# Optimization experiments

Hardware: AMD Instinct MI355X
Metric: run time of the kernel (lower is better)

The kernel has to match this reference:

```python
import jax, jax.numpy as jnp
import numpy as np

B, T = 16, 2048
D_EMB, D_CND2, H_RNN, H_FC, N_OUT = 256, 640, 896, 1024, 1024


def setup_inputs() -> dict:
    key = jax.random.key(0)
    ks = jax.random.split(key, 12)
    s = 0.02
    return {
        "reference_sample": jax.random.randint(ks[0], (B, T), 0, N_OUT),
        "i_cnd_series": jax.random.normal(ks[1], (B, T, D_CND2), dtype=jnp.float32),
        "emb": jax.random.normal(ks[2], (N_OUT, D_EMB), dtype=jnp.float32) * s,
        "W_ih": jax.random.normal(ks[3], (3 * H_RNN, D_EMB + D_CND2), dtype=jnp.float32) * s,
        "b_ih": jnp.zeros((3 * H_RNN,), jnp.float32),
        "W_hh": jax.random.normal(ks[4], (3 * H_RNN, H_RNN), dtype=jnp.float32) * s,
        "b_hh": jnp.zeros((3 * H_RNN,), jnp.float32),
        "fc1_w": jax.random.normal(ks[5], (H_FC, H_RNN), dtype=jnp.float32) * s,
        "fc1_b": jnp.zeros((H_FC,), jnp.float32),
        "fc2_w": jax.random.normal(ks[6], (N_OUT, H_FC), dtype=jnp.float32) * s,
        "fc2_b": jnp.zeros((N_OUT,), jnp.float32),
    }


def _gru(x, W_ih, b_ih, W_hh, b_hh):
    # x: [B, T, D_in] -> hidden states [B, T, H] (PyTorch GRU gate order r, z, n)
    Bn = x.shape[0]
    gx = jnp.einsum("btd,gd->btg", x, W_ih) + b_ih  # precompute input gates [B,T,3H]
    gx = jnp.transpose(gx, (1, 0, 2))  # [T,B,3H]

    def step(h, gxt):
        gh = h @ W_hh.T + b_hh
        rx, zx, nx = jnp.split(gxt, 3, axis=-1)
        rh, zh, nh = jnp.split(gh, 3, axis=-1)
        r = jax.nn.sigmoid(rx + rh)
        z = jax.nn.sigmoid(zx + zh)
        n = jnp.tanh(nx + r * nh)
        h_new = (1.0 - z) * n + z * h
        return h_new, h_new

    h0 = jnp.zeros((Bn, W_hh.shape[1]), x.dtype)
    _, hs = jax.lax.scan(step, h0, gx)
    return jnp.transpose(hs, (1, 0, 2))  # [B,T,H]


def reference(reference_sample, i_cnd_series, emb, W_ih, b_ih, W_hh, b_hh,
              fc1_w, fc1_b, fc2_w, fc2_b):
    x_emb = emb[reference_sample]                      # [B,T,D_EMB]
    x = jnp.concatenate([x_emb, i_cnd_series], axis=2)  # [B,T,D_EMB+2*cnd]
    o_rnn = _gru(x, W_ih, b_ih, W_hh, b_hh)            # [B,T,H_RNN]
    h = jax.nn.relu(jnp.einsum("bth,fh->btf", o_rnn, fc1_w) + fc1_b)
    return jnp.einsum("btf,of->bto", h, fc2_w) + fc2_b  # [B,T,N_OUT]
```

## Files before the change

kernel.cpp:

```cpp
#include <hip/hip_runtime.h>
#include <hip/hip_bf16.h>

typedef __bf16 bf16;
typedef __bf16 bf16x2 __attribute__((ext_vector_type(2)));
typedef __bf16 bf16x8 __attribute__((ext_vector_type(8)));
typedef float  floatx4 __attribute__((ext_vector_type(4)));

#define NWG 56

static constexpr size_t FL_OFF  = 0;
static constexpr size_t HB_OFF  = 8192;
static constexpr size_t WBF_OFF = 65536;
static constexpr size_t GX_OFF  = WBF_OFF + 13565952;
static constexpr size_t HSX_OFF = GX_OFF + 176160768;

static constexpr size_t W_IH_E = 2688 * 896;
static constexpr size_t W_HH_E = 2688 * 896;
static constexpr size_t W_F1_E = 1024 * 896;

__device__ __forceinline__ float sigm(float x)      { return 1.f / (1.f + __expf(-x)); }
__device__ __forceinline__ float fast_tanh(float x) { return 2.f / (1.f + __expf(-2.f * x)) - 1.f; }

__global__ __launch_bounds__(256) void k_cvt(const float* __restrict__ src,
                                             bf16* __restrict__ dst)
{
    const int s = blockIdx.x * 256 + threadIdx.x;
    const float4 a = ((const float4*)src)[s * 2 + 0];
    const float4 b = ((const float4*)src)[s * 2 + 1];
    bf16x8 v;
    v[0] = (bf16)a.x; v[1] = (bf16)a.y; v[2] = (bf16)a.z; v[3] = (bf16)a.w;
    v[4] = (bf16)b.x; v[5] = (bf16)b.y; v[6] = (bf16)b.z; v[7] = (bf16)b.w;
    ((bf16x8*)dst)[s] = v;
}

__global__ __launch_bounds__(256) void k_embed(const int* __restrict__ samp,
                                               const float* __restrict__ cnd,
                                               const float* __restrict__ emb,
                                               bf16* __restrict__ x)
{
    const int s = blockIdx.x * 256 + threadIdx.x;
    const int r = s / 112;
    const int c = s % 112;
    const float* src;
    if (c < 32) src = emb + samp[r] * 256 + c * 8;
    else        src = cnd + (long)r * 640 + (c - 32) * 8;
    const float4 a = ((const float4*)src)[0];
    const float4 b = ((const float4*)src)[1];
    bf16x8 v;
    v[0] = (bf16)a.x; v[1] = (bf16)a.y; v[2] = (bf16)a.z; v[3] = (bf16)a.w;
    v[4] = (bf16)b.x; v[5] = (bf16)b.y; v[6] = (bf16)b.z; v[7] = (bf16)b.w;
    *(bf16x8*)(x + (long)r * 896 + c * 8) = v;
}

template <int RELU, int GXMODE, int OUTF32>
__global__ __launch_bounds__(256, 2) void gemm_bt(const bf16* __restrict__ A,
                                                  const bf16* __restrict__ Bw,
                                                  const float* __restrict__ bias,
                                                  void* __restrict__ Cv,
                                                  int M, int N, int K)
{
    __shared__ bf16 As[128 * 40];
    __shared__ bf16 Bs[128 * 40];

    const int tid  = threadIdx.x;
    const int lane = tid & 63;
    const int wv   = tid >> 6;
    const int wm   = wv >> 1;
    const int wn   = wv & 1;
    const int n16  = lane & 15;
    const int quad = lane >> 4;
    const int tm   = blockIdx.y * 128;
    const int tn   = blockIdx.x * 128;

    floatx4 acc[4][4] = {};

    const int s0 = tid, s1 = tid + 256;
    const int r0 = s0 >> 2, c0 = s0 & 3;
    const int r1 = s1 >> 2, c1 = s1 & 3;

    const int KT = K >> 5;
    for (int kt = 0; kt < KT; ++kt) {
        const int k0 = kt * 32;
        bf16x8 a0 = *(const bf16x8*)(A  + (long)(tm + r0) * K + k0 + c0 * 8);
        bf16x8 a1 = *(const bf16x8*)(A  + (long)(tm + r1) * K + k0 + c1 * 8);
        bf16x8 b0 = *(const bf16x8*)(Bw + (long)(tn + r0) * K + k0 + c0 * 8);
        bf16x8 b1 = *(const bf16x8*)(Bw + (long)(tn + r1) * K + k0 + c1 * 8);
        __syncthreads();
        *(bf16x8*)(As + r0 * 40 + c0 * 8) = a0;
        *(bf16x8*)(As + r1 * 40 + c1 * 8) = a1;
        *(bf16x8*)(Bs + r0 * 40 + c0 * 8) = b0;
        *(bf16x8*)(Bs + r1 * 40 + c1 * 8) = b1;
        __syncthreads();

        bf16x8 af[4], bfj[4];
#pragma unroll
        for (int i = 0; i < 4; ++i)
            af[i] = *(const bf16x8*)(As + (wm * 64 + i * 16 + n16) * 40 + quad * 8);
#pragma unroll
        for (int j = 0; j < 4; ++j)
            bfj[j] = *(const bf16x8*)(Bs + (wn * 64 + j * 16 + n16) * 40 + quad * 8);
#pragma unroll
        for (int i = 0; i < 4; ++i)
#pragma unroll
            for (int j = 0; j < 4; ++j)
                acc[i][j] = __builtin_amdgcn_mfma_f32_16x16x32_bf16(af[i], bfj[j], acc[i][j], 0, 0, 0);
    }

#pragma unroll
    for (int j = 0; j < 4; ++j) {
        const int c = tn + wn * 64 + j * 16 + n16;
        const float bv = bias[c];
#pragma unroll
        for (int i = 0; i < 4; ++i) {
            const int rbase = tm + wm * 64 + i * 16 + quad * 4;
#pragma unroll
            for (int rr = 0; rr < 4; ++rr) {
                float v = acc[i][j][rr] + bv;
                if (RELU) v = fmaxf(v, 0.f);
                const int r = rbase + rr;
                long oidx;
                if (GXMODE) { const int tt = r & 2047, bb = r >> 11; oidx = (long)(tt * 16 + bb) * N + c; }
                else        { oidx = (long)r * N + c; }
                if (OUTF32) ((float*)Cv)[oidx] = v;
                else        ((bf16*)Cv)[oidx]  = (bf16)v;
            }
        }
    }
}

__global__ __launch_bounds__(192, 1) void gru_scan(const bf16* __restrict__ Whh,
                                                   const float* __restrict__ bhh,
                                                   const bf16* __restrict__ gx,
                                                   bf16* __restrict__ hs,
                                                   bf16* __restrict__ hbuf,
                                                   unsigned int* __restrict__ flags)
{
    __shared__ bf16  hst[16 * 904];
    __shared__ float gacc[3][16][16];
    __shared__ float bhs[3][16];

    const int tid  = threadIdx.x;
    const int wv   = tid >> 6;
    const int lane = tid & 63;
    const int n16  = lane & 15;
    const int quad = lane >> 4;
    const int wg   = blockIdx.x;
    const int col0 = wg * 16;

    bf16x8 wf[28];
    {
        const bf16* wrow = Whh + (long)(wv * 896 + col0 + n16) * 896;
#pragma unroll
        for (int kt = 0; kt < 28; ++kt)
            wf[kt] = *(const bf16x8*)(wrow + kt * 32 + quad * 8);
    }
    if (tid < 48) bhs[tid / 16][tid % 16] = bhh[(tid / 16) * 896 + col0 + (tid % 16)];

    const int u0 = tid - 64;
    const int b  = u0 >> 3;
    const int c2 = (u0 & 7) * 2;
    float hl0 = 0.f, hl1 = 0.f;
    float gxv[6];
    if (tid >= 64) {
        const bf16* g0 = gx + (long)(0 * 16 + b) * 2688 + col0 + c2;
#pragma unroll
        for (int g = 0; g < 3; ++g) {
            gxv[g * 2 + 0] = (float)g0[g * 896 + 0];
            gxv[g * 2 + 1] = (float)g0[g * 896 + 1];
        }
    }
    __syncthreads();

    for (int t = 0; t < 2048; ++t) {
        const bf16* hb_cur  = hbuf + (t & 1) * (56 * 256);
        bf16*       hb_next = hbuf + ((t + 1) & 1) * (56 * 256);

        if (tid < 64) {
            if (t > 0) {
                for (;;) {
                    unsigned f = (lane < NWG)
                        ? __hip_atomic_load(flags + lane * 32, __ATOMIC_RELAXED, __HIP_MEMORY_SCOPE_AGENT)
                        : 0xFFFFFFFFu;
                    if (__all(f >= (unsigned)t)) break;
                    __builtin_amdgcn_s_sleep(1);
                }
            }
            __threadfence();
        }
        __syncthreads();

        {
            bf16x8 seg[9];
#pragma unroll
            for (int it = 0; it < 9; ++it)
                seg[it] = *(const bf16x8*)(hb_cur + (tid + it * 192) * 8);
            bf16x8 segl;
            if (tid < 64) segl = *(const bf16x8*)(hb_cur + (1728 + tid) * 8);
#pragma unroll
            for (int it = 0; it < 9; ++it) {
                const int s = tid + it * 192;
                const int ct = s >> 5, rem = s & 31, bb = rem >> 1, hf = rem & 1;
                *(bf16x8*)(hst + bb * 904 + ct * 16 + hf * 8) = seg[it];
            }
            if (tid < 64) {
                const int s = 1728 + tid;
                const int ct = s >> 5, rem = s & 31, bb = rem >> 1, hf = rem & 1;
                *(bf16x8*)(hst + bb * 904 + ct * 16 + hf * 8) = segl;
            }
        }
        __syncthreads();

        floatx4 acc = {0.f, 0.f, 0.f, 0.f};
#pragma unroll
        for (int kt = 0; kt < 28; ++kt) {
            bf16x8 af = *(const bf16x8*)(hst + n16 * 904 + kt * 32 + quad * 8);
            acc = __builtin_amdgcn_mfma_f32_16x16x32_bf16(af, wf[kt], acc, 0, 0, 0);
        }
#pragma unroll
        for (int r = 0; r < 4; ++r) gacc[wv][quad * 4 + r][n16] = acc[r];
        __syncthreads();

        if (tid >= 64) {
            float hn[2];
            const float hold[2] = { hl0, hl1 };
#pragma unroll
            for (int u = 0; u < 2; ++u) {
                const int c = c2 + u;
                const float ghr = gacc[0][b][c] + bhs[0][c];
                const float ghz = gacc[1][b][c] + bhs[1][c];
                const float ghn = gacc[2][b][c] + bhs[2][c];
                const float rg = sigm(gxv[0 + u] + ghr);
                const float zg = sigm(gxv[2 + u] + ghz);
                const float ng = fast_tanh(gxv[4 + u] + rg * ghn);
                hn[u] = (1.f - zg) * ng + zg * hold[u];
            }
            hl0 = hn[0]; hl1 = hn[1];
            bf16x2 hv; hv[0] = (bf16)hn[0]; hv[1] = (bf16)hn[1];
            *(bf16x2*)(hb_next + wg * 256 + b * 16 + c2) = hv;
            *(bf16x2*)(hs + ((long)b * 2048 + t) * 896 + col0 + c2) = hv;
        }
        __syncthreads();

        if (tid == 0) {
            __threadfence();
            __hip_atomic_store(flags + wg * 32, (unsigned)(t + 1),
                               __ATOMIC_RELEASE, __HIP_MEMORY_SCOPE_AGENT);
        }

        if (tid >= 64) {
            const int tn_ = (t + 1 < 2048) ? (t + 1) : 2047;
            const bf16* g0 = gx + (long)(tn_ * 16 + b) * 2688 + col0 + c2;
#pragma unroll
            for (int g = 0; g < 3; ++g) {
                gxv[g * 2 + 0] = (float)g0[g * 896 + 0];
                gxv[g * 2 + 1] = (float)g0[g * 896 + 1];
            }
        }
    }
}

extern "C" void kernel_launch(void* const* d_in, const int* in_sizes, int n_in,
                              void* d_out, int out_size, void* d_ws, size_t ws_size,
                              hipStream_t stream)
{
    const int*   samp = (const int*)d_in[0];
    const float* cnd  = (const float*)d_in[1];
    const float* emb  = (const float*)d_in[2];
    const float* Wih  = (const float*)d_in[3];
    const float* bih  = (const float*)d_in[4];
    const float* Whh  = (const float*)d_in[5];
    const float* bhh  = (const float*)d_in[6];
    const float* fc1w = (const float*)d_in[7];
    const float* fc1b = (const float*)d_in[8];
    const float* fc2w = (const float*)d_in[9];
    const float* fc2b = (const float*)d_in[10];

    char* ws = (char*)d_ws;
    unsigned int* flags = (unsigned int*)(ws + FL_OFF);
    bf16* hbuf = (bf16*)(ws + HB_OFF);
    bf16* wbf  = (bf16*)(ws + WBF_OFF);
    bf16* gx   = (bf16*)(ws + GX_OFF);
    bf16* hs   = (bf16*)(ws + HSX_OFF);
    bf16* x    = (bf16*)(ws + HSX_OFF);
    bf16* h1   = (bf16*)(ws + GX_OFF);

    bf16* wih_bf = wbf;
    bf16* whh_bf = wbf + W_IH_E;
    bf16* fc1_bf = whh_bf + W_HH_E;
    bf16* fc2_bf = fc1_bf + W_F1_E;

    (void)hipMemsetAsync(flags, 0, 8192, stream);
    (void)hipMemsetAsync(hbuf, 0, 57344, stream);

    k_cvt<<<1176, 256, 0, stream>>>(Wih,  wih_bf);
    k_cvt<<<1176, 256, 0, stream>>>(Whh,  whh_bf);
    k_cvt<<< 448, 256, 0, stream>>>(fc1w, fc1_bf);
    k_cvt<<< 512, 256, 0, stream>>>(fc2w, fc2_bf);

    k_embed<<<14336, 256, 0, stream>>>(samp, cnd, emb, x);
    gemm_bt<0, 1, 0><<<dim3(21, 256), 256, 0, stream>>>(x, wih_bf, bih, gx, 32768, 2688, 896);
    gru_scan<<<NWG, 192, 0, stream>>>(whh_bf, bhh, gx, hs, hbuf, flags);
    gemm_bt<1, 0, 0><<<dim3(8, 256), 256, 0, stream>>>(hs, fc1_bf, fc1b, h1, 32768, 1024, 896);
    gemm_bt<0, 0, 1><<<dim3(8, 256), 256, 0, stream>>>(h1, fc2_bf, fc2b, d_out, 32768, 1024, 1024);
}
```

Before: 11.97 ms.

## Collapse GRU scan workgroup to a single wave with register-resident gates

The recurrent scan kernel now runs one 64-lane wave per workgroup instead of three waves. That wave holds all three gate weight slices in registers and computes the r/z/n MFMAs itself, reading h directly from global memory in row-major layout. This removes the LDS staging of h, the shared-memory gate exchange and the several __syncthreads per timestep on the serial critical path. In exchange it uses heavy VGPR pressure (84 bf16x8 weight fragments), each wave does three times the MFMA work, and cross-workgroup ordering now relies on relaxed atomic stores plus s_waitcnt and an acquire fence.

```diff
diff --git a/kernel.cpp b/kernel.cpp
--- a/kernel.cpp
+++ b/kernel.cpp
@@ -20,6 +20,19 @@
 
 __device__ __forceinline__ float sigm(float x)      { return 1.f / (1.f + __expf(-x)); }
 __device__ __forceinline__ float fast_tanh(float x) { return 2.f / (1.f + __expf(-2.f * x)) - 1.f; }
+
+__device__ __forceinline__ unsigned pack_bf2(float lo, float hi)
+{
+    union { bf16x2 v; unsigned u; } cv;
+    cv.v[0] = (bf16)lo; cv.v[1] = (bf16)hi;
+    return cv.u;
+}
+__device__ __forceinline__ unsigned short bf_bits(float x)
+{
+    union { bf16 v; unsigned short u; } cv;
+    cv.v = (bf16)x;
+    return cv.u;
+}
 
 __global__ __launch_bounds__(256) void k_cvt(const float* __restrict__ src,
                                              bf16* __restrict__ dst)
@@ -128,134 +141,117 @@
     }
 }
 
-__global__ __launch_bounds__(192, 1) void gru_scan(const bf16* __restrict__ Whh,
-                                                   const float* __restrict__ bhh,
-                                                   const bf16* __restrict__ gx,
-                                                   bf16* __restrict__ hs,
-                                                   bf16* __restrict__ hbuf,
-                                                   unsigned int* __restrict__ flags)
-{
-    __shared__ bf16  hst[16 * 904];
-    __shared__ float gacc[3][16][16];
-    __shared__ float bhs[3][16];
-
-    const int tid  = threadIdx.x;
-    const int wv   = tid >> 6;
-    const int lane = tid & 63;
+__global__ __launch_bounds__(64, 1) void gru_scan(const bf16* __restrict__ Whh,
+                                                  const float* __restrict__ bhh,
+                                                  const bf16* __restrict__ gx,
+                                                  bf16* __restrict__ hs,
+                                                  bf16* __restrict__ hbuf,
+                                                  unsigned int* __restrict__ flags)
+{
+    const int lane = threadIdx.x;
     const int n16  = lane & 15;
     const int quad = lane >> 4;
     const int wg   = blockIdx.x;
     const int col0 = wg * 16;
-
-    bf16x8 wf[28];
+    const int c    = col0 + n16;
+
+    bf16x8 wfr[28], wfz[28], wfn[28];
     {
-        const bf16* wrow = Whh + (long)(wv * 896 + col0 + n16) * 896;
-#pragma unroll
-        for (int kt = 0; kt < 28; ++kt)
-            wf[kt] = *(const bf16x8*)(wrow + kt * 32 + quad * 8);
+        const bf16* w0 = Whh + (long)(0 * 896 + c) * 896 + quad * 8;
+        const bf16* w1 = Whh + (long)(1 * 896 + c) * 896 + quad * 8;
+        const bf16* w2 = Whh + (long)(2 * 896 + c) * 896 + quad * 8;
+#pragma unroll
+        for (int kt = 0; kt < 28; ++kt) {
+            wfr[kt] = *(const bf16x8*)(w0 + kt * 32);
+            wfz[kt] = *(const bf16x8*)(w1 + kt * 32);
+            wfn[kt] = *(const bf16x8*)(w2 + kt * 32);
+        }
     }
-    if (tid < 48) bhs[tid / 16][tid % 16] = bhh[(tid / 16) * 896 + col0 + (tid % 16)];
-
-    const int u0 = tid - 64;
-    const int b  = u0 >> 3;
-    const int c2 = (u0 & 7) * 2;
-    float hl0 = 0.f, hl1 = 0.f;
-    float gxv[6];
-    if (tid >= 64) {
-        const bf16* g0 = gx + (long)(0 * 16 + b) * 2688 + col0 + c2;
-#pragma unroll
-        for (int g = 0; g < 3; ++g) {
-            gxv[g * 2 + 0] = (float)g0[g * 896 + 0];
-            gxv[g * 2 + 1] = (float)g0[g * 896 + 1];
-        }
-    }
-    __syncthreads();
+    const float bhr = bhh[0 * 896 + c];
+    const float bhz = bhh[1 * 896 + c];
+    const float bhn = bhh[2 * 896 + c];
+
+    float hl[4] = {0.f, 0.f, 0.f, 0.f};
+
+    float gxv[12];
+#pragma unroll
+    for (int g = 0; g < 3; ++g)
+#pragma unroll
+        for (int rr = 0; rr < 4; ++rr)
+            gxv[g * 4 + rr] = (float)gx[(long)(quad * 4 + rr) * 2688 + g * 896 + c];
 
     for (int t = 0; t < 2048; ++t) {
-        const bf16* hb_cur  = hbuf + (t & 1) * (56 * 256);
-        bf16*       hb_next = hbuf + ((t + 1) & 1) * (56 * 256);
-
-        if (tid < 64) {
-            if (t > 0) {
-                for (;;) {
-                    unsigned f = (lane < NWG)
-                        ? __hip_atomic_load(flags + lane * 32, __ATOMIC_RELAXED, __HIP_MEMORY_SCOPE_AGENT)
-                        : 0xFFFFFFFFu;
-                    if (__all(f >= (unsigned)t)) break;
-                    __builtin_amdgcn_s_sleep(1);
-                }
+        const bf16* hb_cur  = hbuf + (t & 1) * (16 * 896);
+        bf16*       hb_next = hbuf + ((t + 1) & 1) * (16 * 896);
+
+        if (t > 0) {
+            for (;;) {
+                unsigned f = (lane < NWG)
+                    ? __hip_atomic_load(flags + lane * 32, __ATOMIC_RELAXED, __HIP_MEMORY_SCOPE_AGENT)
+                    : 0xFFFFFFFFu;
+                if (__all(f >= (unsigned)t)) break;
+                __builtin_amdgcn_s_sleep(1);
             }
-            __threadfence();
-        }
-        __syncthreads();
+        }
+        __builtin_amdgcn_fence(__ATOMIC_ACQUIRE, "agent");
+
+        floatx4 ar = {0.f, 0.f, 0.f, 0.f};
+        floatx4 az = {0.f, 0.f, 0.f, 0.f};
+        floatx4 an = {0.f, 0.f, 0.f, 0.f};
+        const bf16* hrow = hb_cur + n16 * 896 + quad * 8;
+#pragma unroll
+        for (int kt = 0; kt < 28; ++kt) {
+            bf16x8 af = *(const bf16x8*)(hrow + kt * 32);
+            ar = __builtin_amdgcn_mfma_f32_16x16x32_bf16(af, wfr[kt], ar, 0, 0, 0);
+            az = __builtin_amdgcn_mfma_f32_16x16x32_bf16(af, wfz[kt], az, 0, 0, 0);
+            an = __builtin_amdgcn_mfma_f32_16x16x32_bf16(af, wfn[kt], an, 0, 0, 0);
+        }
+
+        float hn[4];
+#pragma unroll
+        for (int rr = 0; rr < 4; ++rr) {
+            const float rg = sigm(gxv[0 + rr] + ar[rr] + bhr);
+            const float zg = sigm(gxv[4 + rr] + az[rr] + bhz);
+            const float ng = fast_tanh(gxv[8 + rr] + rg * (an[rr] + bhn));
+            hn[rr] = (1.f - zg) * ng + zg * hl[rr];
+            hl[rr] = hn[rr];
+        }
 
         {
-            bf16x8 seg[9];
-#pragma unroll
-            for (int it = 0; it < 9; ++it)
-                seg[it] = *(const bf16x8*)(hb_cur + (tid + it * 192) * 8);
-            bf16x8 segl;
-            if (tid < 64) segl = *(const bf16x8*)(hb_cur + (1728 + tid) * 8);
-#pragma unroll
-            for (int it = 0; it < 9; ++it) {
-                const int s = tid + it * 192;
-                const int ct = s >> 5, rem = s & 31, bb = rem >> 1, hf = rem & 1;
-                *(bf16x8*)(hst + bb * 904 + ct * 16 + hf * 8) = seg[it];
+            unsigned pk[4];
+#pragma unroll
+            for (int rr = 0; rr < 4; ++rr) {
+                const float p  = __shfl_xor(hn[rr], 1);
+                const float lo = (n16 & 1) ? p : hn[rr];
+                const float hi = (n16 & 1) ? hn[rr] : p;
+                pk[rr] = pack_bf2(lo, hi);
             }
-            if (tid < 64) {
-                const int s = 1728 + tid;
-                const int ct = s >> 5, rem = s & 31, bb = rem >> 1, hf = rem & 1;
-                *(bf16x8*)(hst + bb * 904 + ct * 16 + hf * 8) = segl;
+            const int ceven = col0 + (n16 & ~1);
+            unsigned int* hb32 = (unsigned int*)hb_next;
+            const int rs = (n16 & 1) ? 2 : 0;
+#pragma unroll
+            for (int k = 0; k < 2; ++k) {
+                const int b = quad * 4 + rs + k;
+                __hip_atomic_store(hb32 + ((b * 896 + ceven) >> 1), pk[rs + k],
+                                   __ATOMIC_RELAXED, __HIP_MEMORY_SCOPE_AGENT);
             }
         }
-        __syncthreads();
-
-        floatx4 acc = {0.f, 0.f, 0.f, 0.f};
-#pragma unroll
-        for (int kt = 0; kt < 28; ++kt) {
-            bf16x8 af = *(const bf16x8*)(hst + n16 * 904 + kt * 32 + quad * 8);
-            acc = __builtin_amdgcn_mfma_f32_16x16x32_bf16(af, wf[kt], acc, 0, 0, 0);
-        }
-#pragma unroll
-        for (int r = 0; r < 4; ++r) gacc[wv][quad * 4 + r][n16] = acc[r];
-        __syncthreads();
-
-        if (tid >= 64) {
-            float hn[2];
-            const float hold[2] = { hl0, hl1 };
-#pragma unroll
-            for (int u = 0; u < 2; ++u) {
-                const int c = c2 + u;
-                const float ghr = gacc[0][b][c] + bhs[0][c];
-                const float ghz = gacc[1][b][c] + bhs[1][c];
-                const float ghn = gacc[2][b][c] + bhs[2][c];
-                const float rg = sigm(gxv[0 + u] + ghr);
-                const float zg = sigm(gxv[2 + u] + ghz);
-                const float ng = fast_tanh(gxv[4 + u] + rg * ghn);
-                hn[u] = (1.f - zg) * ng + zg * hold[u];
-            }
-            hl0 = hn[0]; hl1 = hn[1];
-            bf16x2 hv; hv[0] = (bf16)hn[0]; hv[1] = (bf16)hn[1];
-            *(bf16x2*)(hb_next + wg * 256 + b * 16 + c2) = hv;
-            *(bf16x2*)(hs + ((long)b * 2048 + t) * 896 + col0 + c2) = hv;
-        }
-        __syncthreads();
-
-        if (tid == 0) {
-            __threadfence();
+        asm volatile("s_waitcnt vmcnt(0)" ::: "memory");
+        if (lane == 0)
             __hip_atomic_store(flags + wg * 32, (unsigned)(t + 1),
-                               __ATOMIC_RELEASE, __HIP_MEMORY_SCOPE_AGENT);
-        }
-
-        if (tid >= 64) {
-            const int tn_ = (t + 1 < 2048) ? (t + 1) : 2047;
-            const bf16* g0 = gx + (long)(tn_ * 16 + b) * 2688 + col0 + c2;
-#pragma unroll
-            for (int g = 0; g < 3; ++g) {
-                gxv[g * 2 + 0] = (float)g0[g * 896 + 0];
-                gxv[g * 2 + 1] = (float)g0[g * 896 + 1];
-            }
-        }
+                               __ATOMIC_RELAXED, __HIP_MEMORY_SCOPE_AGENT);
+
+#pragma unroll
+        for (int rr = 0; rr < 4; ++rr) {
+            const long hidx = ((long)(quad * 4 + rr) * 2048 + t) * 896 + c;
+            __builtin_nontemporal_store(bf_bits(hn[rr]), (unsigned short*)(hs + hidx));
+        }
+        const int tn_ = (t + 1 < 2048) ? (t + 1) : 2047;
+#pragma unroll
+        for (int g = 0; g < 3; ++g)
+#pragma unroll
+            for (int rr = 0; rr < 4; ++rr)
+                gxv[g * 4 + rr] = (float)gx[(long)(tn_ * 16 + quad * 4 + rr) * 2688 + g * 896 + c];
     }
 }
 
@@ -299,7 +295,7 @@
 
     k_embed<<<14336, 256, 0, stream>>>(samp, cnd, emb, x);
     gemm_bt<0, 1, 0><<<dim3(21, 256), 256, 0, stream>>>(x, wih_bf, bih, gx, 32768, 2688, 896);
-    gru_scan<<<NWG, 192, 0, stream>>>(whh_bf, bhh, gx, hs, hbuf, flags);
+    gru_scan<<<NWG, 64, 0, stream>>>(whh_bf, bhh, gx, hs, hbuf, flags);
     gemm_bt<1, 0, 0><<<dim3(8, 256), 256, 0, stream>>>(hs, fc1_bf, fc1b, h1, 32768, 1024, 896);
     gemm_bt<0, 0, 1><<<dim3(8, 256), 256, 0, stream>>>(h1, fc2_bf, fc2b, d_out, 32768, 1024, 1024);
 }
```

Result: slower. 20.82 ms (+73.9%).
